# Optimization experiments

Measured on AMD Instinct MI355X. Metric: run time of the kernel, lower is better.

The kernel has to match this reference:

```python
import jax, jax.numpy as jnp
import numpy as np

H = 1024
M = 4096
K = 64            # max_memory_updates_per_step
THRESH = 0.5      # surprise_threshold
EPS = 1e-12


def setup_inputs() -> dict:
    key = jax.random.key(0)
    ks = jax.random.split(key, 5)
    B, S = 4, 2048
    return {
        "hidden_states": jax.random.normal(ks[0], (B, S, H), dtype=jnp.float32),
        "ln_gamma": jnp.ones((H,), jnp.float32),
        "ln_beta": jnp.zeros((H,), jnp.float32),
        "Wq": jax.random.normal(ks[1], (H, H), jnp.float32) * 0.02,
        "bq": jnp.zeros((H,), jnp.float32),
        "Wo": jax.random.normal(ks[2], (H, H), jnp.float32) * 0.02,
        "bo": jnp.zeros((H,), jnp.float32),
        "memory": jax.random.normal(ks[3], (M, H), jnp.float32),
        "importance_scores": jax.random.uniform(ks[4], (M,), jnp.float32),
    }


def _layer_norm(x, g, b):
    mu = jnp.mean(x, axis=-1, keepdims=True)
    var = jnp.mean(jnp.square(x - mu), axis=-1, keepdims=True)
    return (x - mu) * jax.lax.rsqrt(var + EPS) * g + b


def reference(hidden_states, ln_gamma, ln_beta, Wq, bq, Wo, bo, memory, importance_scores):
    # LayerNorm
    norm = _layer_norm(hidden_states, ln_gamma, ln_beta)  # [B,S,H]

    # Surprise measure (detached): mean |x| over hidden dim
    surprise = jnp.mean(jnp.abs(jax.lax.stop_gradient(norm)), axis=-1)  # [B,S]

    # --- surprise-based memory update (buffers; no gradient, training mode) ---
    flat_h = jax.lax.stop_gradient(norm).reshape(-1, H)   # [B*S, H]
    flat_s = surprise.reshape(-1)                          # [B*S]
    # top-K surprises, descending (matches where>thr -> sort desc -> take K)
    top_vals, top_idx = jax.lax.top_k(flat_s, K)
    valid = top_vals > THRESH                              # entries below threshold: no write
    # K slots with smallest importance, ascending importance order
    _, slots = jax.lax.top_k(-importance_scores, K)
    new_rows = flat_h[top_idx]                             # [K, H]
    old_rows = memory[slots]                               # [K, H]
    mem = memory.at[slots].set(jnp.where(valid[:, None], new_rows, old_rows))  # [M,H]

    # --- query memory ---
    q = jnp.einsum("bsh,oh->bso", norm, Wq) + bq           # query_proj
    sim = jnp.einsum("bsh,mh->bsm", q, mem)                # [B,S,M]
    attn = jax.nn.softmax(sim, axis=-1)
    retrieved = jnp.einsum("bsm,mh->bsh", attn, mem)       # [B,S,H]
    mem_out = jnp.einsum("bsh,oh->bso", retrieved, Wo) + bo  # output_proj

    # dropout in eval mode = identity; residual add
    return hidden_states + mem_out
```

## Files before the change

### kernel.cpp

```cpp
#include <hip/hip_runtime.h>

#define H 1024
#define MMEM 4096
#define NTOK 8192
#define KTOP 64
#define FTHRESH 0.5f

typedef _Float16 half8 __attribute__((ext_vector_type(8)));
typedef float vf4 __attribute__((ext_vector_type(4)));

__device__ __forceinline__ short f2h(float x){
  union { _Float16 h; short s; } u; u.h = (_Float16)x; return u.s;
}
__device__ __forceinline__ float h2f(short s){
  union { _Float16 h; short s; } u; u.s = s; return (float)u.h;
}
__device__ __forceinline__ unsigned fkey_of(float x){
  unsigned u = __float_as_uint(x);
  return (u & 0x80000000u) ? ~u : (u | 0x80000000u);
}
__device__ __forceinline__ float val_of(unsigned k){
  unsigned u = (k & 0x80000000u) ? (k & 0x7fffffffu) : ~k;
  return __uint_as_float(u);
}

__device__ __forceinline__ void gload_lds16(const short* g, short* l){
  __builtin_amdgcn_global_load_lds(
      (const __attribute__((address_space(1))) unsigned int*)g,
      (__attribute__((address_space(3))) unsigned int*)l, 16, 0, 0);
}

__global__ __launch_bounds__(256) void ln_kernel(
    const float* __restrict__ hs, const float* __restrict__ g, const float* __restrict__ be,
    short* __restrict__ n16, float* __restrict__ surprise)
{
  int row = blockIdx.x, tid = threadIdx.x;
  long base = (long)row * H;
  float4 x = ((const float4*)(hs + base))[tid];
  float s1 = x.x + x.y + x.z + x.w;
  float s2 = x.x*x.x + x.y*x.y + x.z*x.z + x.w*x.w;
  __shared__ float r1[4], r2[4], r3[4];
  int w = tid >> 6, lane = tid & 63;
  for (int o = 32; o; o >>= 1){ s1 += __shfl_down(s1, o); s2 += __shfl_down(s2, o); }
  if (lane == 0){ r1[w] = s1; r2[w] = s2; }
  __syncthreads();
  float S1 = r1[0]+r1[1]+r1[2]+r1[3];
  float S2 = r2[0]+r2[1]+r2[2]+r2[3];
  float mean = S1 * (1.0f/H);
  float var  = S2 * (1.0f/H) - mean*mean;
  float rinv = rsqrtf(var + 1e-12f);
  float4 gg = ((const float4*)g)[tid];
  float4 bb = ((const float4*)be)[tid];
  float4 n;
  n.x = (x.x-mean)*rinv*gg.x + bb.x;
  n.y = (x.y-mean)*rinv*gg.y + bb.y;
  n.z = (x.z-mean)*rinv*gg.z + bb.z;
  n.w = (x.w-mean)*rinv*gg.w + bb.w;
  float sa = fabsf(n.x)+fabsf(n.y)+fabsf(n.z)+fabsf(n.w);
  for (int o = 32; o; o >>= 1) sa += __shfl_down(sa, o);
  if (lane == 0) r3[w] = sa;
  __syncthreads();
  if (tid == 0) surprise[row] = (r3[0]+r3[1]+r3[2]+r3[3]) * (1.0f/H);
  short4 h4;
  h4.x = f2h(n.x); h4.y = f2h(n.y); h4.z = f2h(n.z); h4.w = f2h(n.w);
  ((short4*)(n16 + base))[tid] = h4;
}

__global__ __launch_bounds__(256) void topk_local(
    const float* __restrict__ surprise, const float* __restrict__ imp,
    unsigned long long* __restrict__ cand_s, unsigned long long* __restrict__ cand_i)
{
  __shared__ unsigned long long s[256];
  int b = blockIdx.x, tid = threadIdx.x;
  int maxmode = (b < 32);
  int gidx = maxmode ? (b*256 + tid) : ((b-32)*256 + tid);
  float x = maxmode ? surprise[gidx] : imp[gidx];
  unsigned k = fkey_of(x);
  if (!maxmode) k = ~k;
  s[tid] = ((unsigned long long)k << 32) | (unsigned)(8191 - gidx);
  __syncthreads();
  for (int kk = 2; kk <= 256; kk <<= 1)
    for (int j = kk >> 1; j > 0; j >>= 1){
      int i = tid, ixj = i ^ j;
      if (ixj > i){
        bool asc = ((i & kk) == 0);
        unsigned long long a = s[i], c = s[ixj];
        if ((a < c) == asc){ s[i] = c; s[ixj] = a; }
      }
      __syncthreads();
    }
  if (tid < 64){
    if (maxmode) cand_s[b*64 + tid] = s[tid];
    else         cand_i[(b-32)*64 + tid] = s[tid];
  }
}

__global__ __launch_bounds__(256) void topk_merge(
    const unsigned long long* __restrict__ cand_s, const unsigned long long* __restrict__ cand_i,
    float* __restrict__ top_vals, int* __restrict__ top_idx, int* __restrict__ slots)
{
  __shared__ unsigned long long s[2048];
  int tid = threadIdx.x;
  int N = (blockIdx.x == 0) ? 2048 : 1024;
  const unsigned long long* src = (blockIdx.x == 0) ? cand_s : cand_i;
  for (int i = tid; i < N; i += 256) s[i] = src[i];
  __syncthreads();
  for (int kk = 2; kk <= N; kk <<= 1)
    for (int j = kk >> 1; j > 0; j >>= 1){
      for (int i = tid; i < N; i += 256){
        int ixj = i ^ j;
        if (ixj > i){
          bool asc = ((i & kk) == 0);
          unsigned long long a = s[i], c = s[ixj];
          if ((a < c) == asc){ s[i] = c; s[ixj] = a; }
        }
      }
      __syncthreads();
    }
  if (tid < 64){
    unsigned long long p = s[tid];
    int gi = 8191 - (int)(p & 0xffffffffu);
    if (blockIdx.x == 0){
      top_vals[tid] = val_of((unsigned)(p >> 32));
      top_idx[tid] = gi;
    } else {
      slots[tid] = gi;
    }
  }
}

__global__ __launch_bounds__(256) void prep_all_kernel(
    const float* __restrict__ mem, const float* __restrict__ Wq, const float* __restrict__ Wo,
    short* __restrict__ m16, short* __restrict__ memT,
    short* __restrict__ wq_h, short* __restrict__ wq_l, short* __restrict__ wo16)
{
  __shared__ __align__(16) short t[64][66];
  int b = blockIdx.x, tid = threadIdx.x;
  if (b < 1024){
    int r0 = (b >> 4) * 64, c0 = (b & 15) * 64;
    #pragma unroll
    for (int k = 0; k < 4; ++k){
      int idx = k*256 + tid;
      int r = idx >> 4, c4 = (idx & 15) * 4;
      float4 x = *(const float4*)&mem[(long)(r0+r)*H + c0 + c4];
      short4 h;
      h.x = f2h(x.x); h.y = f2h(x.y); h.z = f2h(x.z); h.w = f2h(x.w);
      *(short4*)&m16[(long)(r0+r)*H + c0 + c4] = h;
      t[r][c4] = h.x; t[r][c4+1] = h.y; t[r][c4+2] = h.z; t[r][c4+3] = h.w;
    }
    __syncthreads();
    #pragma unroll
    for (int k = 0; k < 4; ++k){
      int idx = k*256 + tid;
      int c = idx >> 4, r4 = (idx & 15) * 4;
      short4 h;
      h.x = t[r4][c]; h.y = t[r4+1][c]; h.z = t[r4+2][c]; h.w = t[r4+3][c];
      *(short4*)&memT[(long)(c0+c)*MMEM + r0 + r4] = h;
    }
  } else if (b < 2048){
    long i = (long)(b - 1024) * 256 + tid;
    float4 x = ((const float4*)Wq)[i];
    short4 h, l;
    h.x = f2h(x.x); l.x = f2h(x.x - h2f(h.x));
    h.y = f2h(x.y); l.y = f2h(x.y - h2f(h.y));
    h.z = f2h(x.z); l.z = f2h(x.z - h2f(h.z));
    h.w = f2h(x.w); l.w = f2h(x.w - h2f(h.w));
    ((short4*)wq_h)[i] = h;
    ((short4*)wq_l)[i] = l;
  } else {
    long i = (long)(b - 2048) * 256 + tid;
    float4 x = ((const float4*)Wo)[i];
    short4 h;
    h.x = f2h(x.x); h.y = f2h(x.y); h.z = f2h(x.z); h.w = f2h(x.w);
    ((short4*)wo16)[i] = h;
  }
}

__global__ __launch_bounds__(256) void update_kernel(
    const float* __restrict__ top_vals, const int* __restrict__ top_idx, const int* __restrict__ slots,
    const float* __restrict__ hs, const float* __restrict__ g, const float* __restrict__ be,
    short* __restrict__ m16, short* __restrict__ memT)
{
  int i = blockIdx.x;
  if (top_vals[i] <= FTHRESH) return;
  int s = slots[i], r = top_idx[i];
  int tid = threadIdx.x, w = tid >> 6, lane = tid & 63;
  long base = (long)r * H;
  float4 x = ((const float4*)(hs + base))[tid];
  float s1 = x.x + x.y + x.z + x.w;
  float s2 = x.x*x.x + x.y*x.y + x.z*x.z + x.w*x.w;
  __shared__ float r1[4], r2[4];
  for (int o = 32; o; o >>= 1){ s1 += __shfl_down(s1, o); s2 += __shfl_down(s2, o); }
  if (lane == 0){ r1[w] = s1; r2[w] = s2; }
  __syncthreads();
  float S1 = r1[0]+r1[1]+r1[2]+r1[3];
  float S2 = r2[0]+r2[1]+r2[2]+r2[3];
  float mean = S1 * (1.0f/H);
  float var  = S2 * (1.0f/H) - mean*mean;
  float rinv = rsqrtf(var + 1e-12f);
  float4 gg = ((const float4*)g)[tid];
  float4 bb = ((const float4*)be)[tid];
  short4 h4;
  h4.x = f2h((x.x-mean)*rinv*gg.x + bb.x);
  h4.y = f2h((x.y-mean)*rinv*gg.y + bb.y);
  h4.z = f2h((x.z-mean)*rinv*gg.z + bb.z);
  h4.w = f2h((x.w-mean)*rinv*gg.w + bb.w);
  ((short4*)(m16 + (long)s*H))[tid] = h4;
  long c4 = (long)tid * 4;
  memT[(c4+0)*MMEM + s] = h4.x;
  memT[(c4+1)*MMEM + s] = h4.y;
  memT[(c4+2)*MMEM + s] = h4.z;
  memT[(c4+3)*MMEM + s] = h4.w;
}

__global__ __launch_bounds__(256) void bias_kernel(
    const float* __restrict__ bq, const short* __restrict__ m16, float* __restrict__ biasM)
{
  int tid = threadIdx.x, w = tid >> 6, lane = tid & 63;
  int m = blockIdx.x*4 + w;
  const short* ph = m16 + (long)m*H;
  float s = 0.f;
  for (int j = 0; j < 16; ++j){
    int h = lane + j*64;
    s += bq[h] * h2f(ph[h]);
  }
  for (int o = 32; o; o >>= 1) s += __shfl_down(s, o);
  if (lane == 0) biasM[m] = s;
}

template<int SPLIT, int MODE>
__global__ __launch_bounds__(256) void gemm128(
    const short* __restrict__ A,
    const short* __restrict__ Bh, const short* __restrict__ Bl,
    int K, int N,
    short* __restrict__ O1,
    float* __restrict__ Of, const float* __restrict__ resid, const float* __restrict__ biasN)
{
  __shared__ short sA[128*64];
  __shared__ short sBh[128*64];
  __shared__ short sBl[SPLIT ? 128*64 : 64];
  int tid = threadIdx.x, w = tid >> 6, lane = tid & 63, ln = lane & 15, quad = lane >> 4;
  int wr = w >> 1, wc = w & 1;
  int nwgx = gridDim.x;
  int nwg  = nwgx * gridDim.y;
  int lin  = blockIdx.y * nwgx + blockIdx.x;
  int nl   = (lin & 7) * (nwg >> 3) + (lin >> 3);
  long m0 = (long)(nl / nwgx) * 128, n0 = (long)(nl % nwgx) * 128;
  long Kl = K;
  vf4 acc[4][4];
  #pragma unroll
  for (int i = 0; i < 4; ++i) for (int j = 0; j < 4; ++j) for (int r = 0; r < 4; ++r) acc[i][j][r] = 0.0f;

  for (long kk = 0; kk < Kl; kk += 64){
    #pragma unroll
    for (int j = 0; j < 4; ++j){
      int f = (w*4 + j)*64 + lane;
      int row = f >> 3, c8 = f & 7;
      long go = kk + (long)((c8 ^ (row & 7)) * 8);
      gload_lds16(A  + (m0+row)*Kl + go, sA  + (w*4+j)*512);
      gload_lds16(Bh + (n0+row)*Kl + go, sBh + (w*4+j)*512);
      if (SPLIT) gload_lds16(Bl + (n0+row)*Kl + go, sBl + (w*4+j)*512);
    }
    __syncthreads();
    #pragma unroll
    for (int ks = 0; ks < 64; ks += 32){
      int cbase = (ks >> 3) + quad;
      half8 bh[4], bl[4];
      #pragma unroll
      for (int j = 0; j < 4; ++j){
        int rb = wc*64 + j*16 + ln;
        int cb = cbase ^ (rb & 7);
        bh[j] = *(const half8*)&sBh[rb*64 + cb*8];
        if (SPLIT) bl[j] = *(const half8*)&sBl[rb*64 + cb*8];
      }
      #pragma unroll
      for (int i = 0; i < 4; ++i){
        int ra = wr*64 + i*16 + ln;
        int ca = cbase ^ (ra & 7);
        half8 a = *(const half8*)&sA[ra*64 + ca*8];
        #pragma unroll
        for (int j = 0; j < 4; ++j){
          acc[i][j] = __builtin_amdgcn_mfma_f32_16x16x32_f16(a, bh[j], acc[i][j], 0, 0, 0);
          if (SPLIT)
            acc[i][j] = __builtin_amdgcn_mfma_f32_16x16x32_f16(a, bl[j], acc[i][j], 0, 0, 0);
        }
      }
    }
    __syncthreads();
  }

  #pragma unroll
  for (int i = 0; i < 4; ++i){
    #pragma unroll
    for (int j = 0; j < 4; ++j){
      #pragma unroll
      for (int r = 0; r < 4; ++r){
        long row = m0 + wr*64 + i*16 + quad*4 + r;
        long col = n0 + wc*64 + j*16 + ln;
        float v = acc[i][j][r];
        if (MODE == 1){
          O1[row*(long)N + col] = f2h(v + biasN[col]);
        } else if (MODE == 2){
          O1[row*(long)N + col] = f2h(v);
        } else {
          Of[row*(long)N + col] = v + resid[row*(long)N + col] + biasN[col];
        }
      }
    }
  }
}

template<int MODE>
__global__ __launch_bounds__(512, 2) void gemm256(
    const short* __restrict__ A, const short* __restrict__ B,
    int K, int N,
    short* __restrict__ O1, float* __restrict__ Of,
    const float* __restrict__ resid, const float* __restrict__ biasN)
{
  extern __shared__ short lds[];
  int tid = threadIdx.x, w = tid >> 6, lane = tid & 63, ln = lane & 15, quad = lane >> 4;
  int wr = w >> 2, wc = w & 3;
  int nwgx = gridDim.x, nwg = nwgx * gridDim.y;
  int lin = blockIdx.y * nwgx + blockIdx.x;
  int nl  = (lin & 7) * (nwg >> 3) + (lin >> 3);
  long m0 = (long)(nl / nwgx) * 256, n0 = (long)(nl % nwgx) * 256;
  long Kl = K;
  int NT = K >> 6;

  auto STAGE = [&](const short* __restrict__ G, long rowbase, long kt, short* ldsbase){
    #pragma unroll
    for (int i = 0; i < 2; ++i){
      int f = i*512 + tid;
      int row = f >> 3, c8 = f & 7;
      long go = kt + (long)((c8 ^ (row & 7)) * 8);
      gload_lds16(G + (rowbase + row)*Kl + go, ldsbase + i*4096 + w*512);
    }
  };
  auto LOADA = [&](half8 (&af)[4][2], const short* sAh){
    #pragma unroll
    for (int ks = 0; ks < 2; ++ks){
      int cbase = ks*4 + quad;
      #pragma unroll
      for (int i = 0; i < 4; ++i){
        int ra = wr*64 + i*16 + ln;
        af[i][ks] = *(const half8*)&sAh[ra*64 + (cbase ^ (ra & 7))*8];
      }
    }
  };
  auto LOADB = [&](half8 (&bf)[2][2], const short* sBh){
    #pragma unroll
    for (int ks = 0; ks < 2; ++ks){
      int cbase = ks*4 + quad;
      #pragma unroll
      for (int j = 0; j < 2; ++j){
        int rb = wc*32 + j*16 + ln;
        bf[j][ks] = *(const half8*)&sBh[rb*64 + (cbase ^ (rb & 7))*8];
      }
    }
  };

  vf4 acc[4][4][2];
  #pragma unroll
  for (int p = 0; p < 4; ++p)
    for (int i = 0; i < 4; ++i)
      for (int j = 0; j < 2; ++j)
        for (int r = 0; r < 4; ++r) acc[p][i][j][r] = 0.0f;

  {
    int t1 = (NT > 1) ? 1 : 0;
    STAGE(A, m0 + 0,   0, lds + 0);
    STAGE(B, n0 + 0,   0, lds + 16384);
    STAGE(B, n0 + 128, 0, lds + 16384 + 8192);
    STAGE(A, m0 + 128, 0, lds + 8192);
    STAGE(A, m0 + 0,   (long)t1*64, lds + 32768);
    STAGE(B, n0 + 0,   (long)t1*64, lds + 32768 + 16384);
  }
  asm volatile("s_waitcnt vmcnt(8)" ::: "memory");
  asm volatile("s_barrier" ::: "memory");

  #define PH_PRE()  do { \
    asm volatile("s_barrier" ::: "memory"); \
    asm volatile("s_waitcnt lgkmcnt(0)" ::: "memory"); \
    __builtin_amdgcn_sched_barrier(0); \
    __builtin_amdgcn_s_setprio(1); } while(0)
  #define PH_POST() do { \
    __builtin_amdgcn_s_setprio(0); \
    asm volatile("s_waitcnt vmcnt(8)" ::: "memory"); \
    asm volatile("s_barrier" ::: "memory"); } while(0)
  #define MFMA16(ap, af, bf) do { \
    _Pragma("unroll") \
    for (int i = 0; i < 4; ++i){ \
      _Pragma("unroll") \
      for (int j = 0; j < 2; ++j){ \
        ap[i][j] = __builtin_amdgcn_mfma_f32_16x16x32_f16(af[i][0], bf[j][0], ap[i][j], 0, 0, 0); \
        ap[i][j] = __builtin_amdgcn_mfma_f32_16x16x32_f16(af[i][1], bf[j][1], ap[i][j], 0, 0, 0); \
      } \
    } } while(0)

  for (int t = 0; t < NT; ++t){
    int cur = t & 1;
    short* bA = lds + cur*32768;
    short* bB = bA + 16384;
    short* oA = lds + (cur^1)*32768;
    short* oB = oA + 16384;
    int t1 = t + 1; if (t1 >= NT) t1 -= NT;
    int t2 = t + 2; if (t2 >= NT) t2 -= NT;
    long kt1 = (long)t1 * 64, kt2 = (long)t2 * 64;
    half8 af[4][2], bf0[2][2], bf1[2][2];

    LOADA(af, bA);
    LOADB(bf0, bB);
    STAGE(B, n0 + 128, kt1, oB + 8192);
    PH_PRE();
    MFMA16(acc[0], af, bf0);
    PH_POST();

    LOADB(bf1, bB + 8192);
    STAGE(A, m0 + 128, kt1, oA + 8192);
    PH_PRE();
    MFMA16(acc[1], af, bf1);
    PH_POST();

    LOADA(af, bA + 8192);
    STAGE(A, m0 + 0, kt2, bA);
    PH_PRE();
    MFMA16(acc[2], af, bf0);
    PH_POST();

    STAGE(B, n0 + 0, kt2, bB);
    PH_PRE();
    MFMA16(acc[3], af, bf1);
    PH_POST();
  }
  #undef PH_PRE
  #undef PH_POST
  #undef MFMA16

  float bn[2][2];
  if (MODE != 2){
    #pragma unroll
    for (int bh = 0; bh < 2; ++bh)
      for (int j = 0; j < 2; ++j)
        bn[bh][j] = biasN[n0 + bh*128 + wc*32 + j*16 + ln];
  }
  #pragma unroll
  for (int p = 0; p < 4; ++p){
    #pragma unroll
    for (int i = 0; i < 4; ++i){
      #pragma unroll
      for (int j = 0; j < 2; ++j){
        #pragma unroll
        for (int r = 0; r < 4; ++r){
          long row = m0 + (p >> 1)*128 + wr*64 + i*16 + quad*4 + r;
          long col = n0 + (p & 1)*128 + wc*32 + j*16 + ln;
          float v = acc[p][i][j][r];
          if (MODE == 1){
            O1[row*(long)N + col] = f2h(v + bn[p & 1][j]);
          } else if (MODE == 2){
            O1[row*(long)N + col] = f2h(v);
          } else {
            Of[row*(long)N + col] = v + resid[row*(long)N + col] + bn[p & 1][j];
          }
        }
      }
    }
  }
}

__global__ __launch_bounds__(256) void softmax_kernel(short* __restrict__ simP)
{
  long row = blockIdx.x;
  int tid = threadIdx.x, w = tid >> 6, lane = tid & 63;
  half8* ptr = (half8*)(simP + row*MMEM);
  float xf[16];
  float mx = -1e30f;
  #pragma unroll
  for (int j = 0; j < 2; ++j){
    half8 x = ptr[tid + j*256];
    #pragma unroll
    for (int e = 0; e < 8; ++e){ float f = (float)x[e]; xf[j*8+e] = f; mx = fmaxf(mx, f); }
  }
  for (int o = 32; o; o >>= 1) mx = fmaxf(mx, __shfl_xor(mx, o));
  __shared__ float rmax[4], rsum[4];
  if (lane == 0) rmax[w] = mx;
  __syncthreads();
  mx = fmaxf(fmaxf(rmax[0], rmax[1]), fmaxf(rmax[2], rmax[3]));
  float p[16], s = 0.f;
  #pragma unroll
  for (int k = 0; k < 16; ++k){ p[k] = __expf(xf[k] - mx); s += p[k]; }
  for (int o = 32; o; o >>= 1) s += __shfl_xor(s, o);
  if (lane == 0) rsum[w] = s;
  __syncthreads();
  float inv = 1.0f / (rsum[0]+rsum[1]+rsum[2]+rsum[3]);
  #pragma unroll
  for (int j = 0; j < 2; ++j){
    half8 o8;
    #pragma unroll
    for (int e = 0; e < 8; ++e) o8[e] = (_Float16)(p[j*8+e] * inv);
    ptr[tid + j*256] = o8;
  }
}

extern "C" void kernel_launch(void* const* d_in, const int* in_sizes, int n_in,
                              void* d_out, int out_size, void* d_ws, size_t ws_size,
                              hipStream_t stream)
{
  const float* hs  = (const float*)d_in[0];
  const float* gam = (const float*)d_in[1];
  const float* bet = (const float*)d_in[2];
  const float* Wq  = (const float*)d_in[3];
  const float* bq  = (const float*)d_in[4];
  const float* Wo  = (const float*)d_in[5];
  const float* bo  = (const float*)d_in[6];
  const float* mem = (const float*)d_in[7];
  const float* imp = (const float*)d_in[8];
  float* out = (float*)d_out;

  char* ws = (char*)d_ws;
  short* n16   = (short*)(ws);
  short* q16   = (short*)(ws + (16ull<<20));
  short* m16   = (short*)(ws + (32ull<<20));
  short* memT  = (short*)(ws + (40ull<<20));
  short* simP  = (short*)(ws + (48ull<<20));
  short* vwoT  = (short*)(ws + (112ull<<20));
  short* wq_h  = (short*)(ws + (128ull<<20));
  short* wq_l  = (short*)(ws + (130ull<<20));
  short* wo16  = (short*)(ws + (132ull<<20));
  char*  tail  = ws + (134ull<<20);
  float* biasM    = (float*)tail;
  float* surprise = (float*)(tail + (64<<10));
  float* top_vals = (float*)(tail + (128<<10));
  int*   top_idx  = (int*)  (tail + (129<<10));
  int*   slots    = (int*)  (tail + (130<<10));
  unsigned long long* cand_s = (unsigned long long*)(tail + (132<<10));
  unsigned long long* cand_i = (unsigned long long*)(tail + (148<<10));

  static bool attr_done = false;
  if (!attr_done){
    hipFuncSetAttribute(reinterpret_cast<const void*>(&gemm256<1>),
                        hipFuncAttributeMaxDynamicSharedMemorySize, 131072);
    attr_done = true;
  }

  ln_kernel<<<NTOK, 256, 0, stream>>>(hs, gam, bet, n16, surprise);
  topk_local<<<48, 256, 0, stream>>>(surprise, imp, cand_s, cand_i);
  topk_merge<<<2, 256, 0, stream>>>(cand_s, cand_i, top_vals, top_idx, slots);
  prep_all_kernel<<<3072, 256, 0, stream>>>(mem, Wq, Wo, m16, memT, wq_h, wq_l, wo16);
  update_kernel<<<KTOP, 256, 0, stream>>>(top_vals, top_idx, slots, hs, gam, bet, m16, memT);
  bias_kernel<<<1024, 256, 0, stream>>>(bq, m16, biasM);
  gemm128<0,2><<<dim3(32,8), 256, 0, stream>>>(
      wo16, m16, m16, H, MMEM, vwoT, nullptr, nullptr, nullptr);
  gemm128<2,2><<<dim3(8,64), 256, 0, stream>>>(
      n16, wq_h, wq_l, H, H, q16, nullptr, nullptr, nullptr);
  gemm256<1><<<dim3(16,32), 512, 131072, stream>>>(
      q16, m16, H, MMEM, simP, nullptr, nullptr, biasM);
  softmax_kernel<<<NTOK, 256, 0, stream>>>(simP);
  gemm128<0,3><<<dim3(8,64), 256, 0, stream>>>(
      simP, vwoT, vwoT, MMEM, H, nullptr, out, hs, bo);
}
```

Before: 416.6 us.

## Reassociate query projection into memory: precompute G = mem·Wq instead of Q = norm·Wq

Instead of projecting all 8192 normalized tokens through Wq with a split-precision (hi/lo) GEMM, the code now multiplies the 4096 memory rows by Wq once, giving G = mem·Wq. The similarity GEMM then uses the normalized tokens directly against G. This roughly halves the projection GEMM work and drops the Wq hi/lo split. It also removes the unused transposed-memory buffer and its scattered writes in the update kernel. The trade-off is that the single-fp16 Wq and a reassociated product change rounding in the similarity logits, which softmax could amplify.

```diff
diff --git a/kernel.cpp b/kernel.cpp
--- a/kernel.cpp
+++ b/kernel.cpp
@@ -131,22 +131,34 @@
 
 __global__ __launch_bounds__(256) void prep_all_kernel(
     const float* __restrict__ mem, const float* __restrict__ Wq, const float* __restrict__ Wo,
-    short* __restrict__ m16, short* __restrict__ memT,
-    short* __restrict__ wq_h, short* __restrict__ wq_l, short* __restrict__ wo16)
-{
-  __shared__ __align__(16) short t[64][66];
+    short* __restrict__ m16, short* __restrict__ wqT, short* __restrict__ wo16)
+{
   int b = blockIdx.x, tid = threadIdx.x;
-  if (b < 1024){
-    int r0 = (b >> 4) * 64, c0 = (b & 15) * 64;
+  if (b < 4096){
+    long i = (long)b * 256 + tid;
+    float4 x = ((const float4*)mem)[i];
+    short4 h;
+    h.x = f2h(x.x); h.y = f2h(x.y); h.z = f2h(x.z); h.w = f2h(x.w);
+    ((short4*)m16)[i] = h;
+  } else if (b < 5120){
+    long i = (long)(b - 4096) * 256 + tid;
+    float4 x = ((const float4*)Wo)[i];
+    short4 h;
+    h.x = f2h(x.x); h.y = f2h(x.y); h.z = f2h(x.z); h.w = f2h(x.w);
+    ((short4*)wo16)[i] = h;
+  } else {
+    __shared__ __align__(16) short t[64][66];
+    int tb = b - 5120;
+    int r0 = (tb >> 4) * 64, c0 = (tb & 15) * 64;
     #pragma unroll
     for (int k = 0; k < 4; ++k){
       int idx = k*256 + tid;
       int r = idx >> 4, c4 = (idx & 15) * 4;
-      float4 x = *(const float4*)&mem[(long)(r0+r)*H + c0 + c4];
-      short4 h;
-      h.x = f2h(x.x); h.y = f2h(x.y); h.z = f2h(x.z); h.w = f2h(x.w);
-      *(short4*)&m16[(long)(r0+r)*H + c0 + c4] = h;
-      t[r][c4] = h.x; t[r][c4+1] = h.y; t[r][c4+2] = h.z; t[r][c4+3] = h.w;
+      float4 x = *(const float4*)&Wq[(long)(r0+r)*H + c0 + c4];
+      t[r][c4]   = f2h(x.x);
+      t[r][c4+1] = f2h(x.y);
+      t[r][c4+2] = f2h(x.z);
+      t[r][c4+3] = f2h(x.w);
     }
     __syncthreads();
     #pragma unroll
@@ -155,31 +167,15 @@
       int c = idx >> 4, r4 = (idx & 15) * 4;
       short4 h;
       h.x = t[r4][c]; h.y = t[r4+1][c]; h.z = t[r4+2][c]; h.w = t[r4+3][c];
-      *(short4*)&memT[(long)(c0+c)*MMEM + r0 + r4] = h;
-    }
-  } else if (b < 2048){
-    long i = (long)(b - 1024) * 256 + tid;
-    float4 x = ((const float4*)Wq)[i];
-    short4 h, l;
-    h.x = f2h(x.x); l.x = f2h(x.x - h2f(h.x));
-    h.y = f2h(x.y); l.y = f2h(x.y - h2f(h.y));
-    h.z = f2h(x.z); l.z = f2h(x.z - h2f(h.z));
-    h.w = f2h(x.w); l.w = f2h(x.w - h2f(h.w));
-    ((short4*)wq_h)[i] = h;
-    ((short4*)wq_l)[i] = l;
-  } else {
-    long i = (long)(b - 2048) * 256 + tid;
-    float4 x = ((const float4*)Wo)[i];
-    short4 h;
-    h.x = f2h(x.x); h.y = f2h(x.y); h.z = f2h(x.z); h.w = f2h(x.w);
-    ((short4*)wo16)[i] = h;
+      *(short4*)&wqT[(long)(c0+c)*H + r0 + r4] = h;
+    }
   }
 }
 
 __global__ __launch_bounds__(256) void update_kernel(
     const float* __restrict__ top_vals, const int* __restrict__ top_idx, const int* __restrict__ slots,
     const float* __restrict__ hs, const float* __restrict__ g, const float* __restrict__ be,
-    short* __restrict__ m16, short* __restrict__ memT)
+    short* __restrict__ m16)
 {
   int i = blockIdx.x;
   if (top_vals[i] <= FTHRESH) return;
@@ -206,11 +202,6 @@
   h4.z = f2h((x.z-mean)*rinv*gg.z + bb.z);
   h4.w = f2h((x.w-mean)*rinv*gg.w + bb.w);
   ((short4*)(m16 + (long)s*H))[tid] = h4;
-  long c4 = (long)tid * 4;
-  memT[(c4+0)*MMEM + s] = h4.x;
-  memT[(c4+1)*MMEM + s] = h4.y;
-  memT[(c4+2)*MMEM + s] = h4.z;
-  memT[(c4+3)*MMEM + s] = h4.w;
 }
 
 __global__ __launch_bounds__(256) void bias_kernel(
@@ -518,13 +509,11 @@
 
   char* ws = (char*)d_ws;
   short* n16   = (short*)(ws);
-  short* q16   = (short*)(ws + (16ull<<20));
+  short* g16   = (short*)(ws + (16ull<<20));
   short* m16   = (short*)(ws + (32ull<<20));
-  short* memT  = (short*)(ws + (40ull<<20));
+  short* wqT   = (short*)(ws + (40ull<<20));
   short* simP  = (short*)(ws + (48ull<<20));
   short* vwoT  = (short*)(ws + (112ull<<20));
-  short* wq_h  = (short*)(ws + (128ull<<20));
-  short* wq_l  = (short*)(ws + (130ull<<20));
   short* wo16  = (short*)(ws + (132ull<<20));
   char*  tail  = ws + (134ull<<20);
   float* biasM    = (float*)tail;
@@ -537,23 +526,23 @@
 
   static bool attr_done = false;
   if (!attr_done){
-    hipFuncSetAttribute(reinterpret_cast<const void*>(&gemm256<1>),
-                        hipFuncAttributeMaxDynamicSharedMemorySize, 131072);
+    (void)hipFuncSetAttribute(reinterpret_cast<const void*>(&gemm256<1>),
+                              hipFuncAttributeMaxDynamicSharedMemorySize, 131072);
     attr_done = true;
   }
 
   ln_kernel<<<NTOK, 256, 0, stream>>>(hs, gam, bet, n16, surprise);
   topk_local<<<48, 256, 0, stream>>>(surprise, imp, cand_s, cand_i);
   topk_merge<<<2, 256, 0, stream>>>(cand_s, cand_i, top_vals, top_idx, slots);
-  prep_all_kernel<<<3072, 256, 0, stream>>>(mem, Wq, Wo, m16, memT, wq_h, wq_l, wo16);
-  update_kernel<<<KTOP, 256, 0, stream>>>(top_vals, top_idx, slots, hs, gam, bet, m16, memT);
+  prep_all_kernel<<<5376, 256, 0, stream>>>(mem, Wq, Wo, m16, wqT, wo16);
+  update_kernel<<<KTOP, 256, 0, stream>>>(top_vals, top_idx, slots, hs, gam, bet, m16);
   bias_kernel<<<1024, 256, 0, stream>>>(bq, m16, biasM);
   gemm128<0,2><<<dim3(32,8), 256, 0, stream>>>(
       wo16, m16, m16, H, MMEM, vwoT, nullptr, nullptr, nullptr);
-  gemm128<2,2><<<dim3(8,64), 256, 0, stream>>>(
-      n16, wq_h, wq_l, H, H, q16, nullptr, nullptr, nullptr);
+  gemm128<0,2><<<dim3(8,32), 256, 0, stream>>>(
+      m16, wqT, wqT, H, H, g16, nullptr, nullptr, nullptr);
   gemm256<1><<<dim3(16,32), 512, 131072, stream>>>(
-      q16, m16, H, MMEM, simP, nullptr, nullptr, biasM);
+      n16, g16, H, MMEM, simP, nullptr, nullptr, biasM);
   softmax_kernel<<<NTOK, 256, 0, stream>>>(simP);
   gemm128<0,3><<<dim3(8,64), 256, 0, stream>>>(
       simP, vwoT, vwoT, MMEM, H, nullptr, out, hs, bo);
```

Result: faster. 407.3 us (-2.2%).
